# Optimization experiments

Measured on AMD Instinct MI355X. Metric: run time of the kernel, lower is better.

Reference implementation:

```python
import jax, jax.numpy as jnp
import numpy as np

B, S, H = 1, 2048, 1024
E, F, K = 8, 3584, 2


def setup_inputs() -> dict:
    key = jax.random.key(0)
    ks = jax.random.split(key, 5)
    scale_h = 1.0 / np.sqrt(H)
    scale_f = 1.0 / np.sqrt(F)
    return {
        "hidden_states": jax.random.normal(ks[0], (B, S, H), dtype=jnp.float32),
        "gate_w": jax.random.normal(ks[1], (E, H), dtype=jnp.float32) * scale_h,
        "w1": jax.random.normal(ks[2], (E, F, H), dtype=jnp.float32) * scale_h,
        "w2": jax.random.normal(ks[3], (E, H, F), dtype=jnp.float32) * scale_f,
        "w3": jax.random.normal(ks[4], (E, F, H), dtype=jnp.float32) * scale_h,
    }


def reference(hidden_states, gate_w, w1, w2, w3):
    b, s, h = hidden_states.shape
    x = hidden_states.reshape(-1, h)                      # [T, H]
    T = x.shape[0]
    router_logits = x @ gate_w.T                          # [T, E]
    probs = jax.nn.softmax(router_logits.astype(jnp.float32), axis=-1)
    rw, sel = jax.lax.top_k(probs, K)                     # [T, K]
    rw = rw / jnp.sum(rw, axis=-1, keepdims=True)
    rw = rw.astype(x.dtype)
    # combine weights per (token, expert): scatter top-k routing weights
    combine = jnp.zeros((T, E), dtype=x.dtype).at[
        jnp.arange(T)[:, None], sel
    ].add(rw)                                             # [T, E]
    out = jnp.zeros_like(x)
    for e in range(E):  # small fixed expert count
        # SwiGLU expert FFN (F.linear: x @ W.T)
        hmid = jax.nn.silu(x @ w1[e].T) * (x @ w3[e].T)   # [T, F]
        out = out + combine[:, e:e + 1] * (hmid @ w2[e].T)
    return out.reshape(b, s, h), router_logits
```

## Files before the change

kernel.cpp:

```cpp
#include <hip/hip_runtime.h>
#include <hip/hip_bf16.h>
#include <math.h>

namespace {
constexpr int kT = 2048;
constexpr int kH = 1024;
constexpr int kE = 8;
constexpr int kF = 3584;
constexpr int kK = 2;

constexpr size_t OFF_CNT  = 0;
constexpr size_t OFF_LIST = 1024;
constexpr size_t OFF_RW   = OFF_LIST + sizeof(int) * kE * kT;
constexpr size_t OFF_HMID = 1u << 20;

typedef __attribute__((ext_vector_type(8))) short bf16x8;
typedef __attribute__((ext_vector_type(4))) float fx4;
}

__device__ __forceinline__ short f2bf_s(float f) {
  union { __hip_bfloat16 h; short s; } u;
  u.h = __float2bfloat16(f);
  return u.s;
}

__device__ __forceinline__ bf16x8 pack8(float4 a, float4 b) {
  bf16x8 r;
  r[0] = f2bf_s(a.x); r[1] = f2bf_s(a.y);
  r[2] = f2bf_s(a.z); r[3] = f2bf_s(a.w);
  r[4] = f2bf_s(b.x); r[5] = f2bf_s(b.y);
  r[6] = f2bf_s(b.z); r[7] = f2bf_s(b.w);
  return r;
}

__device__ __forceinline__ int swz(int row, int u) {
  return row * 64 + ((u ^ (row & 7)) << 3);
}

__global__ __launch_bounds__(256) void router_kernel(
    const float* __restrict__ x, const float* __restrict__ gw,
    float* __restrict__ logits_out, int* __restrict__ cnt,
    int* __restrict__ list, float* __restrict__ rw) {
  const int t = blockIdx.x;
  const float* xt = x + (size_t)t * kH;
  __shared__ float lg[kE];
  const int wave = threadIdx.x >> 6;
  const int lane = threadIdx.x & 63;
  for (int e = wave; e < kE; e += 4) {
    const float* g = gw + (size_t)e * kH;
    float s = 0.f;
    for (int h = lane; h < kH; h += 64) s += xt[h] * g[h];
#pragma unroll
    for (int off = 32; off > 0; off >>= 1) s += __shfl_down(s, off, 64);
    if (lane == 0) lg[e] = s;
  }
  __syncthreads();
  if (threadIdx.x < kE) logits_out[(size_t)t * kE + threadIdx.x] = lg[threadIdx.x];
  if (threadIdx.x == 0) {
    float m = lg[0];
#pragma unroll
    for (int e = 1; e < kE; ++e) m = fmaxf(m, lg[e]);
    float p[kE];
#pragma unroll
    for (int e = 0; e < kE; ++e) p[e] = expf(lg[e] - m);
    int i0 = 0;
#pragma unroll
    for (int e = 1; e < kE; ++e) if (p[e] > p[i0]) i0 = e;
    int i1 = (i0 == 0) ? 1 : 0;
#pragma unroll
    for (int e = 0; e < kE; ++e)
      if (e != i0 && e != i1 && p[e] > p[i1]) i1 = e;
    const float w0 = p[i0], w1v = p[i1];
    const float inv = 1.f / (w0 + w1v);
    rw[t * kK + 0] = w0 * inv;
    rw[t * kK + 1] = w1v * inv;
    const int s0 = atomicAdd(&cnt[i0], 1);
    list[i0 * kT + s0] = t * kK + 0;
    const int s1 = atomicAdd(&cnt[i1], 1);
    list[i1 * kT + s1] = t * kK + 1;
  }
}

struct StageM { float4 a[2][2], b1[2][2], b3[2][2]; };

__global__ __launch_bounds__(256) void moe_mid_mfma(
    const float* __restrict__ x, const float* __restrict__ w1,
    const float* __restrict__ w3, const int* __restrict__ cnt,
    const int* __restrict__ list, unsigned short* __restrict__ hmid) {
  const int e = blockIdx.z;
  const int n = cnt[e];
  const int t0 = blockIdx.y * 64;
  if (t0 >= n) return;
  const int f0 = blockIdx.x * 64;

  __shared__ short As[2][64 * 64];
  __shared__ short B1s[2][64 * 64];
  __shared__ short B3s[2][64 * 64];
  __shared__ int ppid[64];
  __shared__ int ptok[64];

  const int tid = threadIdx.x;
  if (tid < 64) {
    const int idx = t0 + tid;
    const int pid = (idx < n) ? list[e * kT + idx] : -1;
    ppid[tid] = pid;
    ptok[tid] = (pid < 0) ? 0 : (pid >> 1);
  }
  __syncthreads();

  const float* w1e = w1 + (size_t)e * kF * kH;
  const float* w3e = w3 + (size_t)e * kF * kH;

  const float* a_src[2]; const float* b1_src[2]; const float* b3_src[2];
  int sw_[2];
#pragma unroll
  for (int i = 0; i < 2; ++i) {
    const int flat = tid + 256 * i;
    const int row = flat >> 3, u = flat & 7;
    a_src[i]  = x + (size_t)ptok[row] * kH + u * 8;
    b1_src[i] = w1e + (size_t)(f0 + row) * kH + u * 8;
    b3_src[i] = w3e + (size_t)(f0 + row) * kH + u * 8;
    sw_[i] = swz(row, u);
  }

  const int lane = tid & 63, wid = tid >> 6;
  const int wr = wid >> 1, wc = wid & 1;
  const int lr = lane & 15, lq = lane >> 4;

  fx4 acc1[2][2], acc3[2][2];
#pragma unroll
  for (int i = 0; i < 2; ++i)
#pragma unroll
    for (int j = 0; j < 2; ++j) { acc1[i][j] = (fx4)(0.f); acc3[i][j] = (fx4)(0.f); }

  auto LOAD = [&](StageM& S, int k0) {
#pragma unroll
    for (int i = 0; i < 2; ++i) {
      S.a[i][0]  = *reinterpret_cast<const float4*>(a_src[i] + k0);
      S.a[i][1]  = *reinterpret_cast<const float4*>(a_src[i] + k0 + 4);
      S.b1[i][0] = *reinterpret_cast<const float4*>(b1_src[i] + k0);
      S.b1[i][1] = *reinterpret_cast<const float4*>(b1_src[i] + k0 + 4);
      S.b3[i][0] = *reinterpret_cast<const float4*>(b3_src[i] + k0);
      S.b3[i][1] = *reinterpret_cast<const float4*>(b3_src[i] + k0 + 4);
    }
  };
  auto STORE = [&](const StageM& S, int buf) {
#pragma unroll
    for (int i = 0; i < 2; ++i) {
      *reinterpret_cast<bf16x8*>(&As[buf][sw_[i]])  = pack8(S.a[i][0], S.a[i][1]);
      *reinterpret_cast<bf16x8*>(&B1s[buf][sw_[i]]) = pack8(S.b1[i][0], S.b1[i][1]);
      *reinterpret_cast<bf16x8*>(&B3s[buf][sw_[i]]) = pack8(S.b3[i][0], S.b3[i][1]);
    }
  };
  auto MFMA_PHASE = [&](int buf) {
    const short* Ab = As[buf]; const short* B1b = B1s[buf]; const short* B3b = B3s[buf];
    __builtin_amdgcn_s_setprio(1);
#pragma unroll
    for (int ks = 0; ks < 2; ++ks) {
      bf16x8 a[2], bb1[2], bb3[2];
#pragma unroll
      for (int mi = 0; mi < 2; ++mi)
        a[mi] = *reinterpret_cast<const bf16x8*>(&Ab[swz(wr * 32 + mi * 16 + lr, ks * 4 + lq)]);
#pragma unroll
      for (int ni = 0; ni < 2; ++ni) {
        bb1[ni] = *reinterpret_cast<const bf16x8*>(&B1b[swz(wc * 32 + ni * 16 + lr, ks * 4 + lq)]);
        bb3[ni] = *reinterpret_cast<const bf16x8*>(&B3b[swz(wc * 32 + ni * 16 + lr, ks * 4 + lq)]);
      }
#pragma unroll
      for (int mi = 0; mi < 2; ++mi)
#pragma unroll
        for (int ni = 0; ni < 2; ++ni) {
          acc1[mi][ni] = __builtin_amdgcn_mfma_f32_16x16x32_bf16(a[mi], bb1[ni], acc1[mi][ni], 0, 0, 0);
          acc3[mi][ni] = __builtin_amdgcn_mfma_f32_16x16x32_bf16(a[mi], bb3[ni], acc3[mi][ni], 0, 0, 0);
        }
    }
    __builtin_amdgcn_s_setprio(0);
  };

  StageM R0, R1;
  constexpr int NIT = kH / 64;
  LOAD(R0, 0);
  LOAD(R1, 64);
  STORE(R0, 0);
  __syncthreads();
#pragma unroll 2
  for (int it = 0; it < NIT; ++it) {
    if (it & 1) {
      if (it + 2 < NIT) LOAD(R1, (it + 2) * 64);
      MFMA_PHASE(1);
      if (it + 1 < NIT) STORE(R0, 0);
    } else {
      if (it + 2 < NIT) LOAD(R0, (it + 2) * 64);
      MFMA_PHASE(0);
      if (it + 1 < NIT) STORE(R1, 1);
    }
    __syncthreads();
  }

#pragma unroll
  for (int mi = 0; mi < 2; ++mi)
#pragma unroll
    for (int i = 0; i < 4; ++i) {
      const int row = wr * 32 + mi * 16 + lq * 4 + i;
      const int pid = ppid[row];
      if (pid < 0) continue;
#pragma unroll
      for (int ni = 0; ni < 2; ++ni) {
        const int col = f0 + wc * 32 + ni * 16 + lr;
        const float s1 = acc1[mi][ni][i];
        const float s3 = acc3[mi][ni][i];
        const float h = s1 * s3 / (1.f + expf(-s1));
        hmid[(size_t)pid * kF + col] = (unsigned short)f2bf_s(h);
      }
    }
}

struct StageO { bf16x8 a[2]; float4 b[2][2]; };

__global__ __launch_bounds__(256) void moe_out_mfma(
    const unsigned short* __restrict__ hmid, const float* __restrict__ w2,
    const int* __restrict__ cnt, const int* __restrict__ list,
    const float* __restrict__ rw, float* __restrict__ out) {
  const int e = blockIdx.z;
  const int n = cnt[e];
  const int p0 = blockIdx.y * 64;
  if (p0 >= n) return;
  const int h0 = blockIdx.x * 64;

  __shared__ short As[2][64 * 64];
  __shared__ short Bs[2][64 * 64];
  __shared__ int ppid[64];
  __shared__ int prow[64];

  const int tid = threadIdx.x;
  if (tid < 64) {
    const int idx = p0 + tid;
    const int pid = (idx < n) ? list[e * kT + idx] : -1;
    ppid[tid] = pid;
    prow[tid] = (pid < 0) ? 0 : pid;
  }
  __syncthreads();

  const float* w2e = w2 + (size_t)e * kH * kF;

  const unsigned short* a_src[2]; const float* b_src[2];
  int sw_[2];
#pragma unroll
  for (int i = 0; i < 2; ++i) {
    const int flat = tid + 256 * i;
    const int row = flat >> 3, u = flat & 7;
    a_src[i] = hmid + (size_t)prow[row] * kF + u * 8;
    b_src[i] = w2e + (size_t)(h0 + row) * kF + u * 8;
    sw_[i] = swz(row, u);
  }

  const int lane = tid & 63, wid = tid >> 6;
  const int wr = wid >> 1, wc = wid & 1;
  const int lr = lane & 15, lq = lane >> 4;

  fx4 acc[2][2];
#pragma unroll
  for (int i = 0; i < 2; ++i)
#pragma unroll
    for (int j = 0; j < 2; ++j) acc[i][j] = (fx4)(0.f);

  auto LOAD = [&](StageO& S, int k0) {
#pragma unroll
    for (int i = 0; i < 2; ++i) {
      S.a[i]    = *reinterpret_cast<const bf16x8*>(a_src[i] + k0);
      S.b[i][0] = *reinterpret_cast<const float4*>(b_src[i] + k0);
      S.b[i][1] = *reinterpret_cast<const float4*>(b_src[i] + k0 + 4);
    }
  };
  auto STORE = [&](const StageO& S, int buf) {
#pragma unroll
    for (int i = 0; i < 2; ++i) {
      *reinterpret_cast<bf16x8*>(&As[buf][sw_[i]]) = S.a[i];
      *reinterpret_cast<bf16x8*>(&Bs[buf][sw_[i]]) = pack8(S.b[i][0], S.b[i][1]);
    }
  };
  auto MFMA_PHASE = [&](int buf) {
    const short* Ab = As[buf]; const short* Bb = Bs[buf];
    __builtin_amdgcn_s_setprio(1);
#pragma unroll
    for (int ks = 0; ks < 2; ++ks) {
      bf16x8 a[2], b[2];
#pragma unroll
      for (int mi = 0; mi < 2; ++mi)
        a[mi] = *reinterpret_cast<const bf16x8*>(&Ab[swz(wr * 32 + mi * 16 + lr, ks * 4 + lq)]);
#pragma unroll
      for (int ni = 0; ni < 2; ++ni)
        b[ni] = *reinterpret_cast<const bf16x8*>(&Bs[buf][swz(wc * 32 + ni * 16 + lr, ks * 4 + lq)]);
#pragma unroll
      for (int mi = 0; mi < 2; ++mi)
#pragma unroll
        for (int ni = 0; ni < 2; ++ni)
          acc[mi][ni] = __builtin_amdgcn_mfma_f32_16x16x32_bf16(a[mi], b[ni], acc[mi][ni], 0, 0, 0);
    }
    __builtin_amdgcn_s_setprio(0);
  };

  StageO R0, R1;
  constexpr int NIT = kF / 64;
  LOAD(R0, 0);
  LOAD(R1, 64);
  STORE(R0, 0);
  __syncthreads();
#pragma unroll 2
  for (int it = 0; it < NIT; ++it) {
    if (it & 1) {
      if (it + 2 < NIT) LOAD(R1, (it + 2) * 64);
      MFMA_PHASE(1);
      if (it + 1 < NIT) STORE(R0, 0);
    } else {
      if (it + 2 < NIT) LOAD(R0, (it + 2) * 64);
      MFMA_PHASE(0);
      if (it + 1 < NIT) STORE(R1, 1);
    }
    __syncthreads();
  }

#pragma unroll
  for (int mi = 0; mi < 2; ++mi)
#pragma unroll
    for (int i = 0; i < 4; ++i) {
      const int row = wr * 32 + mi * 16 + lq * 4 + i;
      const int pid = ppid[row];
      if (pid < 0) continue;
      const int tok = pid >> 1;
      const float w = rw[pid];
      float* op = out + (size_t)tok * kH + h0 + wc * 32 + lr;
#pragma unroll
      for (int ni = 0; ni < 2; ++ni)
        atomicAdd(&op[ni * 16], w * acc[mi][ni][i]);
    }
}

extern "C" void kernel_launch(void* const* d_in, const int* in_sizes, int n_in,
                              void* d_out, int out_size, void* d_ws,
                              size_t ws_size, hipStream_t stream) {
  (void)in_sizes; (void)n_in; (void)out_size; (void)ws_size;
  const float* x  = (const float*)d_in[0];
  const float* gw = (const float*)d_in[1];
  const float* w1 = (const float*)d_in[2];
  const float* w2 = (const float*)d_in[3];
  const float* w3 = (const float*)d_in[4];

  float* out    = (float*)d_out;
  float* logits = out + (size_t)kT * kH;

  char* ws = (char*)d_ws;
  int*            cnt  = (int*)(ws + OFF_CNT);
  int*            list = (int*)(ws + OFF_LIST);
  float*          rw   = (float*)(ws + OFF_RW);
  unsigned short* hmid = (unsigned short*)(ws + OFF_HMID);

  hipMemsetAsync(out, 0, (size_t)kT * kH * sizeof(float), stream);
  hipMemsetAsync(cnt, 0, kE * sizeof(int), stream);

  router_kernel<<<kT, 256, 0, stream>>>(x, gw, logits, cnt, list, rw);

  dim3 g1(kF / 64, kT / 64, kE);
  moe_mid_mfma<<<g1, 256, 0, stream>>>(x, w1, w3, cnt, list, hmid);

  dim3 g2(kH / 64, kT / 64, kE);
  moe_out_mfma<<<g2, 256, 0, stream>>>(hmid, w2, cnt, list, rw, out);
}
```

Baseline: 342.4 us.

## Pre-cast inputs and weights to bf16 and use direct-to-LDS loads in 128-row GEMMs

Adds a cast kernel that converts x, w1, w3 and w2 from fp32 to bf16 in the workspace on every call. New mid and out expert GEMM kernels use 128-token tiles and load swizzled tiles straight into LDS with global_load_lds. This removes the per-tile fp32 load and convert work inside the GEMMs. In exchange, each call pays a full extra read and write pass over all weights, and the new GEMMs are single-buffered with no software pipelining. The new path runs only when the workspace is large enough, otherwise the old kernels run.

Result: slower. 375.0 us (+9.5%).

```diff
diff --git a/kernel.cpp b/kernel.cpp
--- a/kernel.cpp
+++ b/kernel.cpp
@@ -13,6 +13,11 @@
 constexpr size_t OFF_LIST = 1024;
 constexpr size_t OFF_RW   = OFF_LIST + sizeof(int) * kE * kT;
 constexpr size_t OFF_HMID = 1u << 20;
+constexpr size_t OFF_XB   = 32u << 20;
+constexpr size_t OFF_W1B  = 40u << 20;
+constexpr size_t OFF_W3B  = OFF_W1B + (size_t)kE * kF * kH * 2;
+constexpr size_t OFF_W2B  = OFF_W3B + (size_t)kE * kF * kH * 2;
+constexpr size_t WS_NEED  = OFF_W2B + (size_t)kE * kH * kF * 2;
 
 typedef __attribute__((ext_vector_type(8))) short bf16x8;
 typedef __attribute__((ext_vector_type(4))) float fx4;
@@ -35,6 +40,23 @@
 
 __device__ __forceinline__ int swz(int row, int u) {
   return row * 64 + ((u ^ (row & 7)) << 3);
+}
+
+__device__ __forceinline__ void gload16(const void* g, void* l) {
+  __builtin_amdgcn_global_load_lds(
+      (const __attribute__((address_space(1))) void*)g,
+      (__attribute__((address_space(3))) void*)l, 16, 0, 0);
+}
+
+__global__ __launch_bounds__(256) void cast_bf16_kernel(
+    const float* __restrict__ src, unsigned short* __restrict__ dst, int n8) {
+  int i = blockIdx.x * blockDim.x + threadIdx.x;
+  const int stride = gridDim.x * blockDim.x;
+  for (; i < n8; i += stride) {
+    const float4* s = reinterpret_cast<const float4*>(src + (size_t)i * 8);
+    const float4 v0 = s[0], v1 = s[1];
+    *reinterpret_cast<bf16x8*>(dst + (size_t)i * 8) = pack8(v0, v1);
+  }
 }
 
 __global__ __launch_bounds__(256) void router_kernel(
@@ -79,6 +101,211 @@
     const int s1 = atomicAdd(&cnt[i1], 1);
     list[i1 * kT + s1] = t * kK + 1;
   }
+}
+
+
+__global__ __launch_bounds__(256) void moe_mid_gl(
+    const unsigned short* __restrict__ xb, const unsigned short* __restrict__ w1b,
+    const unsigned short* __restrict__ w3b, const int* __restrict__ cnt,
+    const int* __restrict__ list, unsigned short* __restrict__ hmid) {
+  const int e = blockIdx.z;
+  const int n = cnt[e];
+  const int t0 = blockIdx.y * 128;
+  if (t0 >= n) return;
+  const int f0 = blockIdx.x * 64;
+
+  __shared__ short As[128 * 64];
+  __shared__ short B1s[64 * 64];
+  __shared__ short B3s[64 * 64];
+  __shared__ int ppid[128];
+  __shared__ int ptok[128];
+
+  const int tid = threadIdx.x;
+  if (tid < 128) {
+    const int idx = t0 + tid;
+    const int pid = (idx < n) ? list[e * kT + idx] : -1;
+    ppid[tid] = pid;
+    ptok[tid] = (pid < 0) ? 0 : (pid >> 1);
+  }
+  __syncthreads();
+
+  const unsigned short* w1e = w1b + (size_t)e * kF * kH;
+  const unsigned short* w3e = w3b + (size_t)e * kF * kH;
+
+  const unsigned short* a_src[4];
+#pragma unroll
+  for (int c = 0; c < 4; ++c) {
+    const int flat = tid + 256 * c;
+    const int row = flat >> 3, u = flat & 7;
+    a_src[c] = xb + (size_t)ptok[row] * kH + ((u ^ (row & 7)) * 8);
+  }
+  const unsigned short* b1_src[2]; const unsigned short* b3_src[2];
+#pragma unroll
+  for (int c = 0; c < 2; ++c) {
+    const int flat = tid + 256 * c;
+    const int row = flat >> 3, u = flat & 7;
+    const int co = (u ^ (row & 7)) * 8;
+    b1_src[c] = w1e + (size_t)(f0 + row) * kH + co;
+    b3_src[c] = w3e + (size_t)(f0 + row) * kH + co;
+  }
+
+  const int lane = tid & 63, wid = tid >> 6;
+  const int wr = wid >> 1, wc = wid & 1;
+  const int lr = lane & 15, lq = lane >> 4;
+
+  fx4 acc1[4][2], acc3[4][2];
+#pragma unroll
+  for (int i = 0; i < 4; ++i)
+#pragma unroll
+    for (int j = 0; j < 2; ++j) { acc1[i][j] = (fx4)(0.f); acc3[i][j] = (fx4)(0.f); }
+
+  for (int k0 = 0; k0 < kH; k0 += 64) {
+#pragma unroll
+    for (int c = 0; c < 4; ++c)
+      gload16(a_src[c] + k0, &As[(tid + 256 * c) * 8]);
+#pragma unroll
+    for (int c = 0; c < 2; ++c) {
+      gload16(b1_src[c] + k0, &B1s[(tid + 256 * c) * 8]);
+      gload16(b3_src[c] + k0, &B3s[(tid + 256 * c) * 8]);
+    }
+    __syncthreads();
+
+    __builtin_amdgcn_s_setprio(1);
+#pragma unroll
+    for (int ks = 0; ks < 2; ++ks) {
+      bf16x8 a[4], bb1[2], bb3[2];
+#pragma unroll
+      for (int mi = 0; mi < 4; ++mi)
+        a[mi] = *reinterpret_cast<const bf16x8*>(&As[swz(wr * 64 + mi * 16 + lr, ks * 4 + lq)]);
+#pragma unroll
+      for (int ni = 0; ni < 2; ++ni) {
+        bb1[ni] = *reinterpret_cast<const bf16x8*>(&B1s[swz(wc * 32 + ni * 16 + lr, ks * 4 + lq)]);
+        bb3[ni] = *reinterpret_cast<const bf16x8*>(&B3s[swz(wc * 32 + ni * 16 + lr, ks * 4 + lq)]);
+      }
+#pragma unroll
+      for (int mi = 0; mi < 4; ++mi)
+#pragma unroll
+        for (int ni = 0; ni < 2; ++ni) {
+          acc1[mi][ni] = __builtin_amdgcn_mfma_f32_16x16x32_bf16(a[mi], bb1[ni], acc1[mi][ni], 0, 0, 0);
+          acc3[mi][ni] = __builtin_amdgcn_mfma_f32_16x16x32_bf16(a[mi], bb3[ni], acc3[mi][ni], 0, 0, 0);
+        }
+    }
+    __builtin_amdgcn_s_setprio(0);
+    __syncthreads();
+  }
+
+#pragma unroll
+  for (int mi = 0; mi < 4; ++mi)
+#pragma unroll
+    for (int i = 0; i < 4; ++i) {
+      const int row = wr * 64 + mi * 16 + lq * 4 + i;
+      const int pid = ppid[row];
+      if (pid < 0) continue;
+#pragma unroll
+      for (int ni = 0; ni < 2; ++ni) {
+        const int col = f0 + wc * 32 + ni * 16 + lr;
+        const float s1 = acc1[mi][ni][i];
+        const float s3 = acc3[mi][ni][i];
+        const float h = s1 * s3 / (1.f + expf(-s1));
+        hmid[(size_t)pid * kF + col] = (unsigned short)f2bf_s(h);
+      }
+    }
+}
+
+__global__ __launch_bounds__(256) void moe_out_gl(
+    const unsigned short* __restrict__ hmid, const unsigned short* __restrict__ w2b,
+    const int* __restrict__ cnt, const int* __restrict__ list,
+    const float* __restrict__ rw, float* __restrict__ out) {
+  const int e = blockIdx.z;
+  const int n = cnt[e];
+  const int p0 = blockIdx.y * 128;
+  if (p0 >= n) return;
+  const int h0 = blockIdx.x * 64;
+
+  __shared__ short As[128 * 64];
+  __shared__ short Bs[64 * 64];
+  __shared__ int ppid[128];
+  __shared__ int prow[128];
+
+  const int tid = threadIdx.x;
+  if (tid < 128) {
+    const int idx = p0 + tid;
+    const int pid = (idx < n) ? list[e * kT + idx] : -1;
+    ppid[tid] = pid;
+    prow[tid] = (pid < 0) ? 0 : pid;
+  }
+  __syncthreads();
+
+  const unsigned short* w2e = w2b + (size_t)e * kH * kF;
+
+  const unsigned short* a_src[4];
+#pragma unroll
+  for (int c = 0; c < 4; ++c) {
+    const int flat = tid + 256 * c;
+    const int row = flat >> 3, u = flat & 7;
+    a_src[c] = hmid + (size_t)prow[row] * kF + ((u ^ (row & 7)) * 8);
+  }
+  const unsigned short* b_src[2];
+#pragma unroll
+  for (int c = 0; c < 2; ++c) {
+    const int flat = tid + 256 * c;
+    const int row = flat >> 3, u = flat & 7;
+    b_src[c] = w2e + (size_t)(h0 + row) * kF + ((u ^ (row & 7)) * 8);
+  }
+
+  const int lane = tid & 63, wid = tid >> 6;
+  const int wr = wid >> 1, wc = wid & 1;
+  const int lr = lane & 15, lq = lane >> 4;
+
+  fx4 acc[4][2];
+#pragma unroll
+  for (int i = 0; i < 4; ++i)
+#pragma unroll
+    for (int j = 0; j < 2; ++j) acc[i][j] = (fx4)(0.f);
+
+  for (int k0 = 0; k0 < kF; k0 += 64) {
+#pragma unroll
+    for (int c = 0; c < 4; ++c)
+      gload16(a_src[c] + k0, &As[(tid + 256 * c) * 8]);
+#pragma unroll
+    for (int c = 0; c < 2; ++c)
+      gload16(b_src[c] + k0, &Bs[(tid + 256 * c) * 8]);
+    __syncthreads();
+
+    __builtin_amdgcn_s_setprio(1);
+#pragma unroll
+    for (int ks = 0; ks < 2; ++ks) {
+      bf16x8 a[4], b[2];
+#pragma unroll
+      for (int mi = 0; mi < 4; ++mi)
+        a[mi] = *reinterpret_cast<const bf16x8*>(&As[swz(wr * 64 + mi * 16 + lr, ks * 4 + lq)]);
+#pragma unroll
+      for (int ni = 0; ni < 2; ++ni)
+        b[ni] = *reinterpret_cast<const bf16x8*>(&Bs[swz(wc * 32 + ni * 16 + lr, ks * 4 + lq)]);
+#pragma unroll
+      for (int mi = 0; mi < 4; ++mi)
+#pragma unroll
+        for (int ni = 0; ni < 2; ++ni)
+          acc[mi][ni] = __builtin_amdgcn_mfma_f32_16x16x32_bf16(a[mi], b[ni], acc[mi][ni], 0, 0, 0);
+    }
+    __builtin_amdgcn_s_setprio(0);
+    __syncthreads();
+  }
+
+#pragma unroll
+  for (int mi = 0; mi < 4; ++mi)
+#pragma unroll
+    for (int i = 0; i < 4; ++i) {
+      const int row = wr * 64 + mi * 16 + lq * 4 + i;
+      const int pid = ppid[row];
+      if (pid < 0) continue;
+      const int tok = pid >> 1;
+      const float w = rw[pid];
+      float* op = out + (size_t)tok * kH + h0 + wc * 32 + lr;
+#pragma unroll
+      for (int ni = 0; ni < 2; ++ni)
+        atomicAdd(&op[ni * 16], w * acc[mi][ni][i]);
+    }
 }
 
 struct StageM { float4 a[2][2], b1[2][2], b3[2][2]; };
@@ -290,7 +517,7 @@
         a[mi] = *reinterpret_cast<const bf16x8*>(&Ab[swz(wr * 32 + mi * 16 + lr, ks * 4 + lq)]);
 #pragma unroll
       for (int ni = 0; ni < 2; ++ni)
-        b[ni] = *reinterpret_cast<const bf16x8*>(&Bs[buf][swz(wc * 32 + ni * 16 + lr, ks * 4 + lq)]);
+        b[ni] = *reinterpret_cast<const bf16x8*>(&Bb[swz(wc * 32 + ni * 16 + lr, ks * 4 + lq)]);
 #pragma unroll
       for (int mi = 0; mi < 2; ++mi)
 #pragma unroll
@@ -339,7 +566,7 @@
 extern "C" void kernel_launch(void* const* d_in, const int* in_sizes, int n_in,
                               void* d_out, int out_size, void* d_ws,
                               size_t ws_size, hipStream_t stream) {
-  (void)in_sizes; (void)n_in; (void)out_size; (void)ws_size;
+  (void)in_sizes; (void)n_in; (void)out_size;
   const float* x  = (const float*)d_in[0];
   const float* gw = (const float*)d_in[1];
   const float* w1 = (const float*)d_in[2];
@@ -360,9 +587,29 @@
 
   router_kernel<<<kT, 256, 0, stream>>>(x, gw, logits, cnt, list, rw);
 
-  dim3 g1(kF / 64, kT / 64, kE);
-  moe_mid_mfma<<<g1, 256, 0, stream>>>(x, w1, w3, cnt, list, hmid);
-
-  dim3 g2(kH / 64, kT / 64, kE);
-  moe_out_mfma<<<g2, 256, 0, stream>>>(hmid, w2, cnt, list, rw, out);
-}
+  if (ws_size >= WS_NEED) {
+    unsigned short* xb  = (unsigned short*)(ws + OFF_XB);
+    unsigned short* w1b = (unsigned short*)(ws + OFF_W1B);
+    unsigned short* w3b = (unsigned short*)(ws + OFF_W3B);
+    unsigned short* w2b = (unsigned short*)(ws + OFF_W2B);
+
+    const int nw8 = kE * kF * kH / 8;
+    const int nx8 = kT * kH / 8;
+    cast_bf16_kernel<<<2048, 256, 0, stream>>>(x,  xb,  nx8);
+    cast_bf16_kernel<<<2048, 256, 0, stream>>>(w1, w1b, nw8);
+    cast_bf16_kernel<<<2048, 256, 0, stream>>>(w3, w3b, nw8);
+    cast_bf16_kernel<<<2048, 256, 0, stream>>>(w2, w2b, nw8);
+
+    dim3 g1(kF / 64, kT / 128, kE);
+    moe_mid_gl<<<g1, 256, 0, stream>>>(xb, w1b, w3b, cnt, list, hmid);
+
+    dim3 g2(kH / 64, kT / 128, kE);
+    moe_out_gl<<<g2, 256, 0, stream>>>(hmid, w2b, cnt, list, rw, out);
+  } else {
+    dim3 g1(kF / 64, kT / 64, kE);
+    moe_mid_mfma<<<g1, 256, 0, stream>>>(x, w1, w3, cnt, list, hmid);
+
+    dim3 g2(kH / 64, kT / 64, kE);
+    moe_out_mfma<<<g2, 256, 0, stream>>>(hmid, w2, cnt, list, rw, out);
+  }
+}
```
